# Optimization experiments

Hardware: AMD Instinct MI355X
Metric: run time of the kernel (lower is better)

The kernel has to match this reference:

```python
import jax, jax.numpy as jnp
import numpy as np

N = 4096
IN_F = 512
OUT_F = 512


def setup_inputs() -> dict:
    key = jax.random.key(0)
    k1, k2, k3, k4 = jax.random.split(key, 4)
    x = jax.random.normal(k1, (N, IN_F), dtype=jnp.float32)
    adj = jax.random.uniform(k2, (N, N), dtype=jnp.float32)
    # linear params (torch nn.Linear default init: U(-1/sqrt(fan_in), 1/sqrt(fan_in)))
    bound = 1.0 / np.sqrt(IN_F)
    W = jax.random.uniform(k3, (OUT_F, IN_F), minval=-bound, maxval=bound, dtype=jnp.float32)
    b = jax.random.uniform(k4, (OUT_F,), minval=-bound, maxval=bound, dtype=jnp.float32)
    return {"x": x, "adj": adj, "W": W, "b": b}


def reference(x, adj, W, b):
    # adj_hat = adj + I
    adj_hat = adj + jnp.eye(adj.shape[0], dtype=adj.dtype)
    # deg is diagonal with 1/sqrt(rowsum); deg @ adj @ deg == d[:,None] * adj * d[None,:]
    d = 1.0 / jnp.sqrt(adj_hat.sum(axis=1))  # [N]
    norm_adj = d[:, None] * adj_hat * d[None, :]  # [N, N]
    h = norm_adj @ x  # [N, in_features]
    return h @ W.T + b  # [N, out_features]
```

## Files before the change

### kernel.cpp

```cpp
#include <hip/hip_runtime.h>
#include <cstdint>

#define NN 4096
#define FF 512

typedef short bf16x8 __attribute__((ext_vector_type(8)));
typedef float f32x4 __attribute__((ext_vector_type(4)));

__device__ __forceinline__ uint16_t f2bf(float f) {
    uint32_t u = __builtin_bit_cast(uint32_t, f);
    u += 0x7FFFu + ((u >> 16) & 1u);
    return (uint16_t)(u >> 16);
}
__device__ __forceinline__ float bf2f(uint16_t h) {
    uint32_t u = (uint32_t)h << 16;
    return __builtin_bit_cast(float, u);
}

__global__ __launch_bounds__(256) void k_prep(const float* __restrict__ adj,
                                              float* __restrict__ d,
                                              uint16_t* __restrict__ Abf) {
    const int row  = blockIdx.x * 4 + (threadIdx.x >> 6);
    const int lane = threadIdx.x & 63;
    const float4* p = (const float4*)(adj + (size_t)row * NN);
    float4 v[16];
    float s = 0.f;
#pragma unroll
    for (int i = 0; i < 16; ++i) {
        v[i] = p[lane + i * 64];
        s += (v[i].x + v[i].y) + (v[i].z + v[i].w);
    }
#pragma unroll
    for (int off = 1; off < 64; off <<= 1) s += __shfl_xor(s, off);
    const float di = rsqrtf(s + 1.0f);
    if (lane == 0) d[row] = di;
    uint16_t* outp = Abf + (size_t)row * NN;
#pragma unroll
    for (int i = 0; i < 16; ++i) {
        const int cb = (lane + i * 64) * 4;
        float a0 = v[i].x, a1 = v[i].y, a2 = v[i].z, a3 = v[i].w;
        if (cb + 0 == row) a0 += 1.0f;
        if (cb + 1 == row) a1 += 1.0f;
        if (cb + 2 == row) a2 += 1.0f;
        if (cb + 3 == row) a3 += 1.0f;
        ushort4 o;
        o.x = f2bf(a0); o.y = f2bf(a1); o.z = f2bf(a2); o.w = f2bf(a3);
        *(ushort4*)(outp + cb) = o;
    }
}

__global__ __launch_bounds__(256) void k_xc(const float* __restrict__ x,
                                            uint16_t* __restrict__ xbf) {
    const size_t t4 = (size_t)blockIdx.x * 256 + threadIdx.x;
    float4 v = *(const float4*)(x + t4 * 4);
    ushort4 o;
    o.x = f2bf(v.x); o.y = f2bf(v.y); o.z = f2bf(v.z); o.w = f2bf(v.w);
    *(ushort4*)(xbf + t4 * 4) = o;
}

__global__ __launch_bounds__(256) void k_wc(const float* __restrict__ W,
                                            uint16_t* __restrict__ Wbf) {
    const size_t t4 = (size_t)blockIdx.x * 256 + threadIdx.x;
    float4 v = *(const float4*)(W + t4 * 4);
    ushort4 o;
    o.x = f2bf(v.x); o.y = f2bf(v.y); o.z = f2bf(v.z); o.w = f2bf(v.w);
    *(ushort4*)(Wbf + t4 * 4) = o;
}

__global__ __launch_bounds__(256) void k_zt(const float* __restrict__ z32,
                                            const float* __restrict__ d,
                                            uint16_t* __restrict__ zdT) {
    __shared__ uint16_t t[64][72];
    const int k0 = blockIdx.x * 64;
    const int n0 = blockIdx.y * 64;
    const int tid = threadIdx.x;
    const int r   = tid >> 4;
    const int c4  = tid & 15;
#pragma unroll
    for (int pass = 0; pass < 4; ++pass) {
        const int row = pass * 16 + r;
        float4 v = *(const float4*)(z32 + (size_t)(k0 + row) * FF + n0 + c4 * 4);
        const float dk = d[k0 + row];
        t[c4 * 4 + 0][row] = f2bf(v.x * dk);
        t[c4 * 4 + 1][row] = f2bf(v.y * dk);
        t[c4 * 4 + 2][row] = f2bf(v.z * dk);
        t[c4 * 4 + 3][row] = f2bf(v.w * dk);
    }
    __syncthreads();
#pragma unroll
    for (int pass = 0; pass < 2; ++pass) {
        const int cid = pass * 256 + tid;
        const int n  = cid >> 3;
        const int ch = cid & 7;
        *(uint4*)(zdT + (size_t)(n0 + n) * NN + k0 + ch * 8) = *(const uint4*)&t[n][ch * 8];
    }
}

template <int BM, int BN, int K>
__global__ __launch_bounds__(256, 4) void k_mm(const uint16_t* __restrict__ A,
                                               const uint16_t* __restrict__ Bt,
                                               float* __restrict__ outp) {
    constexpr int NTC   = FF / BN;
    constexpr int NT    = K / 64;
    constexpr int MFR   = BM / 32;
    constexpr int NFR   = BN / 32;
    constexpr int LPT_A = BM / 32;
    constexpr int LPT_B = BN / 32;

    __shared__ uint16_t As[BM * 64];
    __shared__ uint16_t Bs[BN * 64];

    const int id   = blockIdx.x;
    const int mt   = id / NTC;
    const int nt   = id % NTC;
    const int m0 = mt * BM;
    const int n0 = nt * BN;

    const int tid  = threadIdx.x;
    const int w    = tid >> 6;
    const int lane = tid & 63;
    const int wm = w >> 1, wn = w & 1;

    f32x4 acc[MFR][NFR] = {};

    for (int t = 0; t < NT; ++t) {
        const int ktb = t * 64;
#pragma unroll
        for (int i = 0; i < LPT_A; ++i) {
            const int boff = i * 4096 + tid * 16;
            const int row  = boff >> 7;
            const int q    = (boff >> 4) & 7;
            const int c    = q ^ (row & 7);
            const uint16_t* src = A + (size_t)(m0 + row) * K + ktb + c * 8;
            __builtin_amdgcn_global_load_lds(
                (const __attribute__((address_space(1))) void*)src,
                (__attribute__((address_space(3))) void*)&As[boff >> 1],
                16, 0, 0);
        }
#pragma unroll
        for (int i = 0; i < LPT_B; ++i) {
            const int boff = i * 4096 + tid * 16;
            const int row  = boff >> 7;
            const int q    = (boff >> 4) & 7;
            const int c    = q ^ (row & 7);
            const uint16_t* src = Bt + (size_t)(n0 + row) * K + ktb + c * 8;
            __builtin_amdgcn_global_load_lds(
                (const __attribute__((address_space(1))) void*)src,
                (__attribute__((address_space(3))) void*)&Bs[boff >> 1],
                16, 0, 0);
        }
        __syncthreads();
#pragma unroll
        for (int kk = 0; kk < 2; ++kk) {
            const int cl = kk * 4 + (lane >> 4);
            bf16x8 af[MFR], bfr[NFR];
#pragma unroll
            for (int mf = 0; mf < MFR; ++mf) {
                const int r = wm * (MFR * 16) + mf * 16 + (lane & 15);
                af[mf] = *(const bf16x8*)&As[r * 64 + ((cl ^ (r & 7)) << 3)];
            }
#pragma unroll
            for (int nf = 0; nf < NFR; ++nf) {
                const int r = wn * (NFR * 16) + nf * 16 + (lane & 15);
                bfr[nf] = *(const bf16x8*)&Bs[r * 64 + ((cl ^ (r & 7)) << 3)];
            }
#pragma unroll
            for (int mf = 0; mf < MFR; ++mf)
#pragma unroll
                for (int nf = 0; nf < NFR; ++nf)
                    acc[mf][nf] = __builtin_amdgcn_mfma_f32_16x16x32_bf16(
                        af[mf], bfr[nf], acc[mf][nf], 0, 0, 0);
        }
        __syncthreads();
    }

    const int rbase = m0 + wm * (MFR * 16) + ((lane >> 4) << 2);
    const int cbase = n0 + wn * (NFR * 16) + (lane & 15);
#pragma unroll
    for (int mf = 0; mf < MFR; ++mf)
#pragma unroll
        for (int nf = 0; nf < NFR; ++nf) {
            const int col = cbase + nf * 16;
#pragma unroll
            for (int r = 0; r < 4; ++r) {
                const int row = rbase + mf * 16 + r;
                outp[(size_t)row * FF + col] = acc[mf][nf][r];
            }
        }
}

__global__ __launch_bounds__(512, 1) void k_mmx(const uint16_t* __restrict__ A,
                                                const uint16_t* __restrict__ Bt,
                                                uint16_t* __restrict__ parts) {
    constexpr int BM = 256, BN = 128, K = NN;
    constexpr int KSLEN = K / 4;
    constexpr int NT    = KSLEN / 64;

    __shared__ uint16_t As[3][BM * 64];
    __shared__ uint16_t Bs[3][BN * 64];

    const int id   = blockIdx.x;
    const int xcd  = id & 7;
    const int slot = id >> 3;
    const int ks   = xcd >> 1;
    const int mt   = ((slot >> 2) << 1) | (xcd & 1);
    const int nt   = slot & 3;
    const int m0 = mt * BM;
    const int n0 = nt * BN;
    const int k0 = ks * KSLEN;

    const int tid  = threadIdx.x;
    const int w    = tid >> 6;
    const int lane = tid & 63;
    const int wm = w >> 1, wn = w & 1;

    f32x4 acc[4][4] = {};

    auto STAGE = [&](int t, int buf) {
        const int ktb = k0 + t * 64;
#pragma unroll
        for (int i = 0; i < 4; ++i) {
            const int boff = i * 8192 + tid * 16;
            const int row  = boff >> 7;
            const int q    = (boff >> 4) & 7;
            const int c    = q ^ (row & 7);
            const uint16_t* src = A + (size_t)(m0 + row) * K + ktb + c * 8;
            __builtin_amdgcn_global_load_lds(
                (const __attribute__((address_space(1))) void*)src,
                (__attribute__((address_space(3))) void*)&As[buf][boff >> 1],
                16, 0, 0);
        }
#pragma unroll
        for (int i = 0; i < 2; ++i) {
            const int boff = i * 8192 + tid * 16;
            const int row  = boff >> 7;
            const int q    = (boff >> 4) & 7;
            const int c    = q ^ (row & 7);
            const uint16_t* src = Bt + (size_t)(n0 + row) * K + ktb + c * 8;
            __builtin_amdgcn_global_load_lds(
                (const __attribute__((address_space(1))) void*)src,
                (__attribute__((address_space(3))) void*)&Bs[buf][boff >> 1],
                16, 0, 0);
        }
    };

    auto COMPUTE = [&](int buf) {
#pragma unroll
        for (int kk = 0; kk < 2; ++kk) {
            const int cl = kk * 4 + (lane >> 4);
            bf16x8 af[4], bfr[4];
#pragma unroll
            for (int mf = 0; mf < 4; ++mf) {
                const int r = wm * 64 + mf * 16 + (lane & 15);
                af[mf] = *(const bf16x8*)&As[buf][r * 64 + ((cl ^ (r & 7)) << 3)];
            }
#pragma unroll
            for (int nf = 0; nf < 4; ++nf) {
                const int r = wn * 64 + nf * 16 + (lane & 15);
                bfr[nf] = *(const bf16x8*)&Bs[buf][r * 64 + ((cl ^ (r & 7)) << 3)];
            }
#pragma unroll
            for (int mf = 0; mf < 4; ++mf)
#pragma unroll
                for (int nf = 0; nf < 4; ++nf)
                    acc[mf][nf] = __builtin_amdgcn_mfma_f32_16x16x32_bf16(
                        af[mf], bfr[nf], acc[mf][nf], 0, 0, 0);
        }
    };

    STAGE(0, 0);
    STAGE(1, 1);
    int sb = 2, cb = 0;
    for (int t = 0; t < NT; ++t) {
        if (t + 2 < NT) {
            STAGE(t + 2, sb);
            sb = (sb == 2) ? 0 : sb + 1;
            asm volatile("s_waitcnt vmcnt(12)" ::: "memory");
        } else if (t + 2 == NT) {
            asm volatile("s_waitcnt vmcnt(6)" ::: "memory");
        } else {
            asm volatile("s_waitcnt vmcnt(0)" ::: "memory");
        }
        __builtin_amdgcn_s_barrier();
        COMPUTE(cb);
        cb = (cb == 2) ? 0 : cb + 1;
        __builtin_amdgcn_s_barrier();
    }

    uint16_t* dst = parts + (size_t)ks * NN * FF;
    const int rbase = m0 + wm * 64 + ((lane >> 4) << 2);
    const int cbase = n0 + wn * 64 + (lane & 15);
#pragma unroll
    for (int mf = 0; mf < 4; ++mf)
#pragma unroll
        for (int nf = 0; nf < 4; ++nf) {
            const int col = cbase + nf * 16;
#pragma unroll
            for (int r = 0; r < 4; ++r) {
                const int row = rbase + mf * 16 + r;
                dst[(size_t)row * FF + col] = f2bf(acc[mf][nf][r]);
            }
        }
}

__global__ __launch_bounds__(256) void k_red(const uint16_t* __restrict__ parts,
                                             const float* __restrict__ d,
                                             const float* __restrict__ b,
                                             float* __restrict__ out) {
    constexpr size_t STRIDE = (size_t)NN * FF;
    const size_t g   = (size_t)blockIdx.x * 256 + threadIdx.x;
    const int    row = (int)((g * 8) >> 9);
    const int    col = (int)((g * 8) & 511);
    float s[8] = {};
#pragma unroll
    for (int p = 0; p < 4; ++p) {
        ushort4 v0 = *(const ushort4*)(parts + p * STRIDE + g * 8);
        ushort4 v1 = *(const ushort4*)(parts + p * STRIDE + g * 8 + 4);
        s[0] += bf2f(v0.x); s[1] += bf2f(v0.y); s[2] += bf2f(v0.z); s[3] += bf2f(v0.w);
        s[4] += bf2f(v1.x); s[5] += bf2f(v1.y); s[6] += bf2f(v1.z); s[7] += bf2f(v1.w);
    }
    const float di = d[row];
    float4 o0, o1;
    o0.x = s[0] * di + b[col + 0];
    o0.y = s[1] * di + b[col + 1];
    o0.z = s[2] * di + b[col + 2];
    o0.w = s[3] * di + b[col + 3];
    o1.x = s[4] * di + b[col + 4];
    o1.y = s[5] * di + b[col + 5];
    o1.z = s[6] * di + b[col + 6];
    o1.w = s[7] * di + b[col + 7];
    *(float4*)(out + g * 8)     = o0;
    *(float4*)(out + g * 8 + 4) = o1;
}

extern "C" void kernel_launch(void* const* d_in, const int* in_sizes, int n_in,
                              void* d_out, int out_size, void* d_ws, size_t ws_size,
                              hipStream_t stream) {
    const float* x   = (const float*)d_in[0];
    const float* adj = (const float*)d_in[1];
    const float* W   = (const float*)d_in[2];
    const float* b   = (const float*)d_in[3];
    float* out = (float*)d_out;

    char* ws = (char*)d_ws;
    float*    d_    = (float*)ws;
    uint16_t* Abf   = (uint16_t*)(ws + 65536);
    uint16_t* zdT   = Abf + (size_t)NN * NN;
    uint16_t* xbf   = zdT + (size_t)FF * NN;
    uint16_t* Wbf   = xbf + (size_t)NN * FF;
    float*    z32   = (float*)(Wbf + (size_t)FF * FF);
    uint16_t* parts = (uint16_t*)(z32 + (size_t)NN * FF);

    k_wc<<<FF * FF / 1024, 256, 0, stream>>>(W, Wbf);
    k_xc<<<NN * FF / 1024, 256, 0, stream>>>(x, xbf);
    k_prep<<<NN / 4, 256, 0, stream>>>(adj, d_, Abf);
    k_mm<64, 64, FF><<<512, 256, 0, stream>>>(xbf, Wbf, z32);
    k_zt<<<dim3(NN / 64, FF / 64), 256, 0, stream>>>(z32, d_, zdT);
    k_mmx<<<256, 512, 0, stream>>>(Abf, zdT, parts);
    k_red<<<NN * FF / 2048, 256, 0, stream>>>(parts, d_, b, out);
}
```

Before: 68.87 us.

## Retile big GEMM to 128x128 blocks with 32x32 MFMA and double buffering

Replaces the 256x128 tile, 512-thread, triple-buffered split-K GEMM with a 128x128 tile, 256-thread kernel. It is launched as 512 blocks with two blocks per CU, uses 32x32x16 bf16 MFMA instead of 16x16x32, and double buffers LDS. The block-to-XCD mapping is reworked so each XCD owns a contiguous range of M tiles across all N tiles and K splits. The goal is better occupancy and fewer LDS reads per MFMA. In exchange, global loads are reused less per tile and the prefetch depth drops from two stages to one.

```diff
diff --git a/kernel.cpp b/kernel.cpp
--- a/kernel.cpp
+++ b/kernel.cpp
@@ -6,6 +6,7 @@
 
 typedef short bf16x8 __attribute__((ext_vector_type(8)));
 typedef float f32x4 __attribute__((ext_vector_type(4)));
+typedef float f32x16 __attribute__((ext_vector_type(16)));
 
 __device__ __forceinline__ uint16_t f2bf(float f) {
     uint32_t u = __builtin_bit_cast(uint32_t, f);
@@ -189,22 +190,25 @@
         }
 }
 
-__global__ __launch_bounds__(512, 1) void k_mmx(const uint16_t* __restrict__ A,
+__global__ __launch_bounds__(256, 2) void k_mmx(const uint16_t* __restrict__ A,
                                                 const uint16_t* __restrict__ Bt,
                                                 uint16_t* __restrict__ parts) {
-    constexpr int BM = 256, BN = 128, K = NN;
-    constexpr int KSLEN = K / 4;
+    constexpr int BM = 128, BN = 128, K = NN, SPLITK = 4;
+    constexpr int NTC   = FF / BN;
+    constexpr int KSLEN = K / SPLITK;
     constexpr int NT    = KSLEN / 64;
-
-    __shared__ uint16_t As[3][BM * 64];
-    __shared__ uint16_t Bs[3][BN * 64];
+    constexpr int MTX   = (NN / BM) / 8;
+
+    __shared__ uint16_t As[2][BM * 64];
+    __shared__ uint16_t Bs[2][BN * 64];
 
     const int id   = blockIdx.x;
     const int xcd  = id & 7;
     const int slot = id >> 3;
-    const int ks   = xcd >> 1;
-    const int mt   = ((slot >> 2) << 1) | (xcd & 1);
-    const int nt   = slot & 3;
+    const int mt   = xcd * MTX + slot / (NTC * SPLITK);
+    const int rem  = slot % (NTC * SPLITK);
+    const int nt   = rem % NTC;
+    const int ks   = rem / NTC;
     const int m0 = mt * BM;
     const int n0 = nt * BN;
     const int k0 = ks * KSLEN;
@@ -214,13 +218,13 @@
     const int lane = tid & 63;
     const int wm = w >> 1, wn = w & 1;
 
-    f32x4 acc[4][4] = {};
+    f32x16 acc[2][2] = {};
 
     auto STAGE = [&](int t, int buf) {
         const int ktb = k0 + t * 64;
 #pragma unroll
         for (int i = 0; i < 4; ++i) {
-            const int boff = i * 8192 + tid * 16;
+            const int boff = i * 4096 + tid * 16;
             const int row  = boff >> 7;
             const int q    = (boff >> 4) & 7;
             const int c    = q ^ (row & 7);
@@ -231,8 +235,8 @@
                 16, 0, 0);
         }
 #pragma unroll
-        for (int i = 0; i < 2; ++i) {
-            const int boff = i * 8192 + tid * 16;
+        for (int i = 0; i < 4; ++i) {
+            const int boff = i * 4096 + tid * 16;
             const int row  = boff >> 7;
             const int q    = (boff >> 4) & 7;
             const int c    = q ^ (row & 7);
@@ -246,59 +250,52 @@
 
     auto COMPUTE = [&](int buf) {
 #pragma unroll
-        for (int kk = 0; kk < 2; ++kk) {
-            const int cl = kk * 4 + (lane >> 4);
-            bf16x8 af[4], bfr[4];
-#pragma unroll
-            for (int mf = 0; mf < 4; ++mf) {
-                const int r = wm * 64 + mf * 16 + (lane & 15);
+        for (int kk = 0; kk < 4; ++kk) {
+            const int cl = kk * 2 + (lane >> 5);
+            bf16x8 af[2], bfr[2];
+#pragma unroll
+            for (int mf = 0; mf < 2; ++mf) {
+                const int r = wm * 64 + mf * 32 + (lane & 31);
                 af[mf] = *(const bf16x8*)&As[buf][r * 64 + ((cl ^ (r & 7)) << 3)];
             }
 #pragma unroll
-            for (int nf = 0; nf < 4; ++nf) {
-                const int r = wn * 64 + nf * 16 + (lane & 15);
+            for (int nf = 0; nf < 2; ++nf) {
+                const int r = wn * 64 + nf * 32 + (lane & 31);
                 bfr[nf] = *(const bf16x8*)&Bs[buf][r * 64 + ((cl ^ (r & 7)) << 3)];
             }
 #pragma unroll
-            for (int mf = 0; mf < 4; ++mf)
-#pragma unroll
-                for (int nf = 0; nf < 4; ++nf)
-                    acc[mf][nf] = __builtin_amdgcn_mfma_f32_16x16x32_bf16(
+            for (int mf = 0; mf < 2; ++mf)
+#pragma unroll
+                for (int nf = 0; nf < 2; ++nf)
+                    acc[mf][nf] = __builtin_amdgcn_mfma_f32_32x32x16_bf16(
                         af[mf], bfr[nf], acc[mf][nf], 0, 0, 0);
         }
     };
 
     STAGE(0, 0);
-    STAGE(1, 1);
-    int sb = 2, cb = 0;
-    for (int t = 0; t < NT; ++t) {
-        if (t + 2 < NT) {
-            STAGE(t + 2, sb);
-            sb = (sb == 2) ? 0 : sb + 1;
-            asm volatile("s_waitcnt vmcnt(12)" ::: "memory");
-        } else if (t + 2 == NT) {
-            asm volatile("s_waitcnt vmcnt(6)" ::: "memory");
-        } else {
-            asm volatile("s_waitcnt vmcnt(0)" ::: "memory");
-        }
+    for (int t = 0; t < NT - 1; ++t) {
+        STAGE(t + 1, (t + 1) & 1);
+        asm volatile("s_waitcnt vmcnt(8)" ::: "memory");
         __builtin_amdgcn_s_barrier();
-        COMPUTE(cb);
-        cb = (cb == 2) ? 0 : cb + 1;
+        COMPUTE(t & 1);
         __builtin_amdgcn_s_barrier();
     }
+    asm volatile("s_waitcnt vmcnt(0)" ::: "memory");
+    __builtin_amdgcn_s_barrier();
+    COMPUTE((NT - 1) & 1);
 
     uint16_t* dst = parts + (size_t)ks * NN * FF;
-    const int rbase = m0 + wm * 64 + ((lane >> 4) << 2);
-    const int cbase = n0 + wn * 64 + (lane & 15);
-#pragma unroll
-    for (int mf = 0; mf < 4; ++mf)
-#pragma unroll
-        for (int nf = 0; nf < 4; ++nf) {
-            const int col = cbase + nf * 16;
-#pragma unroll
-            for (int r = 0; r < 4; ++r) {
-                const int row = rbase + mf * 16 + r;
-                dst[(size_t)row * FF + col] = f2bf(acc[mf][nf][r]);
+    const int rb = m0 + wm * 64 + ((lane >> 5) << 2);
+    const int cb = n0 + wn * 64 + (lane & 31);
+#pragma unroll
+    for (int mf = 0; mf < 2; ++mf)
+#pragma unroll
+        for (int nf = 0; nf < 2; ++nf) {
+            const int gcol = cb + nf * 32;
+#pragma unroll
+            for (int r = 0; r < 16; ++r) {
+                const int grow = rb + mf * 32 + (r & 3) + ((r >> 2) << 3);
+                dst[(size_t)grow * FF + gcol] = f2bf(acc[mf][nf][r]);
             }
         }
 }
@@ -356,6 +353,6 @@
     k_prep<<<NN / 4, 256, 0, stream>>>(adj, d_, Abf);
     k_mm<64, 64, FF><<<512, 256, 0, stream>>>(xbf, Wbf, z32);
     k_zt<<<dim3(NN / 64, FF / 64), 256, 0, stream>>>(z32, d_, zdT);
-    k_mmx<<<256, 512, 0, stream>>>(Abf, zdT, parts);
+    k_mmx<<<512, 256, 0, stream>>>(Abf, zdT, parts);
     k_red<<<NN * FF / 2048, 256, 0, stream>>>(parts, d_, b, out);
 }
```

Measured after the change: 68.73 us. No clear change (-0.2%).

## Restructure big GEMM into 256x256 tiles with split-K of eight and quarter-step pipeline

Applied to the files above, without the earlier changes.

Replaces the 256x128-tile, split-K=4 GEMM with 256x256 tiles and split-K=8, sized so two blocks can share a CU. Each K-step is loaded in four quarter stages that are interleaved with four MFMA sub-blocks, and MFMA priority is raised around them. Partial sums are stored in the per-thread register layout with wide packed stores, and the reduce kernel un-permutes them while applying the scale and bias. The aim is more data reuse per tile and better overlap of loads with MFMA, at the cost of twice as many partial buffers to reduce and scattered output writes. The partials buffer now reuses the z32 region.

```diff
diff --git a/kernel.cpp b/kernel.cpp
--- a/kernel.cpp
+++ b/kernel.cpp
@@ -12,8 +12,8 @@
     u += 0x7FFFu + ((u >> 16) & 1u);
     return (uint16_t)(u >> 16);
 }
-__device__ __forceinline__ float bf2f(uint16_t h) {
-    uint32_t u = (uint32_t)h << 16;
+__device__ __forceinline__ float bf2f(uint32_t h) {
+    uint32_t u = h << 16;
     return __builtin_bit_cast(float, u);
 }
 
@@ -189,117 +189,143 @@
         }
 }
 
-__global__ __launch_bounds__(512, 1) void k_mmx(const uint16_t* __restrict__ A,
-                                                const uint16_t* __restrict__ Bt,
-                                                uint16_t* __restrict__ parts) {
-    constexpr int BM = 256, BN = 128, K = NN;
-    constexpr int KSLEN = K / 4;
+__global__ __launch_bounds__(512, 2) void k_mmx8(const uint16_t* __restrict__ A,
+                                                 const uint16_t* __restrict__ Bt,
+                                                 uint16_t* __restrict__ parts) {
+    constexpr int K = NN, SPLITK = 8;
+    constexpr int KSLEN = K / SPLITK;
     constexpr int NT    = KSLEN / 64;
-
-    __shared__ uint16_t As[3][BM * 64];
-    __shared__ uint16_t Bs[3][BN * 64];
+    constexpr int NS    = 4 * NT;
+
+    __shared__ uint16_t As[2][2][128 * 64];
+    __shared__ uint16_t Bs[2][2][128 * 64];
 
     const int id   = blockIdx.x;
-    const int xcd  = id & 7;
+    const int ks   = id & 7;
     const int slot = id >> 3;
-    const int ks   = xcd >> 1;
-    const int mt   = ((slot >> 2) << 1) | (xcd & 1);
-    const int nt   = slot & 3;
-    const int m0 = mt * BM;
-    const int n0 = nt * BN;
+    const int mt   = slot >> 1;
+    const int nt   = slot & 1;
+    const int m0 = mt * 256;
+    const int n0 = nt * 256;
     const int k0 = ks * KSLEN;
 
     const int tid  = threadIdx.x;
+    const int lane = tid & 63;
     const int w    = tid >> 6;
-    const int lane = tid & 63;
-    const int wm = w >> 1, wn = w & 1;
-
-    f32x4 acc[4][4] = {};
-
-    auto STAGE = [&](int t, int buf) {
-        const int ktb = k0 + t * 64;
-#pragma unroll
-        for (int i = 0; i < 4; ++i) {
-            const int boff = i * 8192 + tid * 16;
-            const int row  = boff >> 7;
-            const int q    = (boff >> 4) & 7;
-            const int c    = q ^ (row & 7);
-            const uint16_t* src = A + (size_t)(m0 + row) * K + ktb + c * 8;
-            __builtin_amdgcn_global_load_lds(
-                (const __attribute__((address_space(1))) void*)src,
-                (__attribute__((address_space(3))) void*)&As[buf][boff >> 1],
-                16, 0, 0);
-        }
+    const int wm   = w >> 2;
+    const int wn   = w & 3;
+
+    f32x4 acc[8][4] = {};
+
+    auto STAGE = [&](int s) {
+        if (s >= NS) return;
+        const int Ts   = s >> 2;
+        const int hs   = s & 3;
+        const int db   = Ts & 1;
+        const int ktb  = k0 + Ts * 64;
+        const bool isA = (hs == 1) || (hs == 2);
+        const int half = (hs >= 2) ? 1 : 0;
 #pragma unroll
         for (int i = 0; i < 2; ++i) {
             const int boff = i * 8192 + tid * 16;
             const int row  = boff >> 7;
-            const int q    = (boff >> 4) & 7;
-            const int c    = q ^ (row & 7);
-            const uint16_t* src = Bt + (size_t)(n0 + row) * K + ktb + c * 8;
-            __builtin_amdgcn_global_load_lds(
-                (const __attribute__((address_space(1))) void*)src,
-                (__attribute__((address_space(3))) void*)&Bs[buf][boff >> 1],
-                16, 0, 0);
+            const int q8   = (boff >> 4) & 7;
+            const int c    = q8 ^ (row & 7);
+            if (isA) {
+                const uint16_t* src = A + (size_t)(m0 + half * 128 + row) * K + ktb + c * 8;
+                __builtin_amdgcn_global_load_lds(
+                    (const __attribute__((address_space(1))) void*)src,
+                    (__attribute__((address_space(3))) void*)&As[db][half][boff >> 1],
+                    16, 0, 0);
+            } else {
+                const uint16_t* src = Bt + (size_t)(n0 + half * 128 + row) * K + ktb + c * 8;
+                __builtin_amdgcn_global_load_lds(
+                    (const __attribute__((address_space(1))) void*)src,
+                    (__attribute__((address_space(3))) void*)&Bs[db][half][boff >> 1],
+                    16, 0, 0);
+            }
         }
     };
 
-    auto COMPUTE = [&](int buf) {
-#pragma unroll
-        for (int kk = 0; kk < 2; ++kk) {
-            const int cl = kk * 4 + (lane >> 4);
-            bf16x8 af[4], bfr[4];
-#pragma unroll
-            for (int mf = 0; mf < 4; ++mf) {
-                const int r = wm * 64 + mf * 16 + (lane & 15);
-                af[mf] = *(const bf16x8*)&As[buf][r * 64 + ((cl ^ (r & 7)) << 3)];
-            }
-#pragma unroll
-            for (int nf = 0; nf < 4; ++nf) {
-                const int r = wn * 64 + nf * 16 + (lane & 15);
-                bfr[nf] = *(const bf16x8*)&Bs[buf][r * 64 + ((cl ^ (r & 7)) << 3)];
-            }
-#pragma unroll
-            for (int mf = 0; mf < 4; ++mf)
-#pragma unroll
-                for (int nf = 0; nf < 4; ++nf)
-                    acc[mf][nf] = __builtin_amdgcn_mfma_f32_16x16x32_bf16(
-                        af[mf], bfr[nf], acc[mf][nf], 0, 0, 0);
+    auto RD_A = [&](bf16x8* dst, int db, int mh) {
+#pragma unroll
+        for (int mf = 0; mf < 4; ++mf) {
+            const int rr = mh * 64 + mf * 16 + (lane & 15);
+#pragma unroll
+            for (int kk = 0; kk < 2; ++kk) {
+                const int cl = kk * 4 + (lane >> 4);
+                dst[mf * 2 + kk] =
+                    *(const bf16x8*)&As[db][wm][rr * 64 + ((cl ^ (rr & 7)) << 3)];
+            }
         }
     };
-
-    STAGE(0, 0);
-    STAGE(1, 1);
-    int sb = 2, cb = 0;
-    for (int t = 0; t < NT; ++t) {
-        if (t + 2 < NT) {
-            STAGE(t + 2, sb);
-            sb = (sb == 2) ? 0 : sb + 1;
-            asm volatile("s_waitcnt vmcnt(12)" ::: "memory");
-        } else if (t + 2 == NT) {
-            asm volatile("s_waitcnt vmcnt(6)" ::: "memory");
-        } else {
-            asm volatile("s_waitcnt vmcnt(0)" ::: "memory");
-        }
-        __builtin_amdgcn_s_barrier();
-        COMPUTE(cb);
-        cb = (cb == 2) ? 0 : cb + 1;
-        __builtin_amdgcn_s_barrier();
-    }
-
-    uint16_t* dst = parts + (size_t)ks * NN * FF;
-    const int rbase = m0 + wm * 64 + ((lane >> 4) << 2);
-    const int cbase = n0 + wn * 64 + (lane & 15);
-#pragma unroll
-    for (int mf = 0; mf < 4; ++mf)
-#pragma unroll
-        for (int nf = 0; nf < 4; ++nf) {
-            const int col = cbase + nf * 16;
-#pragma unroll
-            for (int r = 0; r < 4; ++r) {
-                const int row = rbase + mf * 16 + r;
-                dst[(size_t)row * FF + col] = f2bf(acc[mf][nf][r]);
-            }
+    auto RD_B = [&](bf16x8* dst, int db, int nh) {
+#pragma unroll
+        for (int nf = 0; nf < 2; ++nf) {
+            const int rr = (wn & 1) * 64 + (nh * 2 + nf) * 16 + (lane & 15);
+#pragma unroll
+            for (int kk = 0; kk < 2; ++kk) {
+                const int cl = kk * 4 + (lane >> 4);
+                dst[nf * 2 + kk] =
+                    *(const bf16x8*)&Bs[db][wn >> 1][rr * 64 + ((cl ^ (rr & 7)) << 3)];
+            }
+        }
+    };
+    auto MM = [&](const bf16x8* a, const bf16x8* b, int mh, int nh) {
+        __builtin_amdgcn_s_setprio(1);
+#pragma unroll
+        for (int mf = 0; mf < 4; ++mf)
+#pragma unroll
+            for (int nf = 0; nf < 2; ++nf)
+#pragma unroll
+                for (int kk = 0; kk < 2; ++kk)
+                    acc[mh * 4 + mf][nh * 2 + nf] = __builtin_amdgcn_mfma_f32_16x16x32_bf16(
+                        a[mf * 2 + kk], b[nf * 2 + kk], acc[mh * 4 + mf][nh * 2 + nf], 0, 0, 0);
+        __builtin_amdgcn_s_setprio(0);
+    };
+
+    STAGE(0); STAGE(1); STAGE(2); STAGE(3); STAGE(4); STAGE(5);
+    asm volatile("s_waitcnt vmcnt(4)" ::: "memory");
+    __builtin_amdgcn_s_barrier();
+
+    for (int T = 0; T < NT; ++T) {
+        const int db = T & 1;
+        bf16x8 a_lo[8], a_hi[8], b_lo[4], b_hi[4];
+        STAGE(4 * T + 6);
+        RD_A(a_lo, db, 0);
+        RD_B(b_lo, db, 0);
+        __builtin_amdgcn_s_barrier();
+        MM(a_lo, b_lo, 0, 0);
+        __builtin_amdgcn_s_barrier();
+        STAGE(4 * T + 7);
+        RD_B(b_hi, db, 1);
+        __builtin_amdgcn_s_barrier();
+        MM(a_lo, b_hi, 0, 1);
+        __builtin_amdgcn_s_barrier();
+        STAGE(4 * T + 8);
+        RD_A(a_hi, db, 1);
+        __builtin_amdgcn_s_barrier();
+        MM(a_hi, b_hi, 1, 1);
+        __builtin_amdgcn_s_barrier();
+        STAGE(4 * T + 9);
+        if (T < NT - 2)       asm volatile("s_waitcnt vmcnt(4)" ::: "memory");
+        else if (T == NT - 2) asm volatile("s_waitcnt vmcnt(0)" ::: "memory");
+        __builtin_amdgcn_s_barrier();
+        MM(a_hi, b_lo, 1, 0);
+        __builtin_amdgcn_s_barrier();
+    }
+
+    uint16_t* dst = parts + ((size_t)id * 512 + tid) * 128;
+#pragma unroll
+    for (int mf = 0; mf < 8; ++mf)
+#pragma unroll
+        for (int nf = 0; nf < 4; nf += 2) {
+            uint32_t w0 = (uint32_t)f2bf(acc[mf][nf][0])     | ((uint32_t)f2bf(acc[mf][nf][1]) << 16);
+            uint32_t w1 = (uint32_t)f2bf(acc[mf][nf][2])     | ((uint32_t)f2bf(acc[mf][nf][3]) << 16);
+            uint32_t w2 = (uint32_t)f2bf(acc[mf][nf + 1][0]) | ((uint32_t)f2bf(acc[mf][nf + 1][1]) << 16);
+            uint32_t w3 = (uint32_t)f2bf(acc[mf][nf + 1][2]) | ((uint32_t)f2bf(acc[mf][nf + 1][3]) << 16);
+            uint4 v = {w0, w1, w2, w3};
+            *(uint4*)(dst + (mf * 4 + nf) * 4) = v;
         }
 }
 
@@ -307,30 +333,46 @@
                                              const float* __restrict__ d,
                                              const float* __restrict__ b,
                                              float* __restrict__ out) {
-    constexpr size_t STRIDE = (size_t)NN * FF;
-    const size_t g   = (size_t)blockIdx.x * 256 + threadIdx.x;
-    const int    row = (int)((g * 8) >> 9);
-    const int    col = (int)((g * 8) & 511);
-    float s[8] = {};
-#pragma unroll
-    for (int p = 0; p < 4; ++p) {
-        ushort4 v0 = *(const ushort4*)(parts + p * STRIDE + g * 8);
-        ushort4 v1 = *(const ushort4*)(parts + p * STRIDE + g * 8 + 4);
-        s[0] += bf2f(v0.x); s[1] += bf2f(v0.y); s[2] += bf2f(v0.z); s[3] += bf2f(v0.w);
-        s[4] += bf2f(v1.x); s[5] += bf2f(v1.y); s[6] += bf2f(v1.z); s[7] += bf2f(v1.w);
-    }
-    const float di = d[row];
-    float4 o0, o1;
-    o0.x = s[0] * di + b[col + 0];
-    o0.y = s[1] * di + b[col + 1];
-    o0.z = s[2] * di + b[col + 2];
-    o0.w = s[3] * di + b[col + 3];
-    o1.x = s[4] * di + b[col + 4];
-    o1.y = s[5] * di + b[col + 5];
-    o1.z = s[6] * di + b[col + 6];
-    o1.w = s[7] * di + b[col + 7];
-    *(float4*)(out + g * 8)     = o0;
-    *(float4*)(out + g * 8 + 4) = o1;
+    const int gid  = blockIdx.x * 256 + threadIdx.x;
+    const int pair = gid >> 2;
+    const int qq   = gid & 3;
+    const int slot = pair >> 9;
+    const int mtid = pair & 511;
+
+    float s[32];
+#pragma unroll
+    for (int i = 0; i < 32; ++i) s[i] = 0.f;
+#pragma unroll
+    for (int ks = 0; ks < 8; ++ks) {
+        const uint16_t* src = parts + ((size_t)(slot * 8 + ks) * 512 + mtid) * 128 + qq * 32;
+        const uint4* sv = (const uint4*)src;
+#pragma unroll
+        for (int j = 0; j < 4; ++j) {
+            uint4 v = sv[j];
+            s[j * 8 + 0] += bf2f(v.x & 0xFFFF); s[j * 8 + 1] += bf2f(v.x >> 16);
+            s[j * 8 + 2] += bf2f(v.y & 0xFFFF); s[j * 8 + 3] += bf2f(v.y >> 16);
+            s[j * 8 + 4] += bf2f(v.z & 0xFFFF); s[j * 8 + 5] += bf2f(v.z >> 16);
+            s[j * 8 + 6] += bf2f(v.w & 0xFFFF); s[j * 8 + 7] += bf2f(v.w >> 16);
+        }
+    }
+
+    const int lane = mtid & 63;
+    const int w    = mtid >> 6;
+    const int wm = w >> 2, wn = w & 3;
+    const int mt = slot >> 1, nt = slot & 1;
+#pragma unroll
+    for (int f = 0; f < 8; ++f) {
+        const int fi = qq * 8 + f;
+        const int mf = fi >> 2, nf = fi & 3;
+        const int gr0 = mt * 256 + wm * 128 + mf * 16 + ((lane >> 4) << 2);
+        const int gc  = nt * 256 + wn * 64 + nf * 16 + (lane & 15);
+        const float bv = b[gc];
+#pragma unroll
+        for (int r = 0; r < 4; ++r) {
+            const int grow = gr0 + r;
+            out[(size_t)grow * FF + gc] = s[f * 4 + r] * d[grow] + bv;
+        }
+    }
 }
 
 extern "C" void kernel_launch(void* const* d_in, const int* in_sizes, int n_in,
@@ -349,13 +391,13 @@
     uint16_t* xbf   = zdT + (size_t)FF * NN;
     uint16_t* Wbf   = xbf + (size_t)NN * FF;
     float*    z32   = (float*)(Wbf + (size_t)FF * FF);
-    uint16_t* parts = (uint16_t*)(z32 + (size_t)NN * FF);
+    uint16_t* parts = (uint16_t*)z32;
 
     k_wc<<<FF * FF / 1024, 256, 0, stream>>>(W, Wbf);
     k_xc<<<NN * FF / 1024, 256, 0, stream>>>(x, xbf);
     k_prep<<<NN / 4, 256, 0, stream>>>(adj, d_, Abf);
     k_mm<64, 64, FF><<<512, 256, 0, stream>>>(xbf, Wbf, z32);
     k_zt<<<dim3(NN / 64, FF / 64), 256, 0, stream>>>(z32, d_, zdT);
-    k_mmx<<<256, 512, 0, stream>>>(Abf, zdT, parts);
-    k_red<<<NN * FF / 2048, 256, 0, stream>>>(parts, d_, b, out);
-}
+    k_mmx8<<<256, 512, 0, stream>>>(Abf, zdT, parts);
+    k_red<<<256, 256, 0, stream>>>(parts, d_, b, out);
+}
```

Result: slower. 77.08 us (+11.9%).
